# Performance work log

Measured on AMD Instinct MI355X. Metric: run time of the kernel, lower is better.

## Reference

```python
import jax, jax.numpy as jnp
import numpy as np

ENC_IN = 21
D_MODEL = 512
E_LAYERS = 2
PRED_LEN = 96
SEQ_LEN = 512
BATCH = 128


def _gru_layer(x, W_ih, W_hh, b_ih, b_hh):
    # x: [B, T, F]; W_ih: [3d, F]; W_hh: [3d, d]; gate order r, z, n (PyTorch)
    B = x.shape[0]
    d = W_hh.shape[1]
    gates_x = jnp.einsum('btf,gf->btg', x, W_ih) + b_ih  # [B, T, 3d], input GEMM hoisted out of scan

    def step(h, gx):
        gh = h @ W_hh.T + b_hh                       # [B, 3d]
        xr, xz, xn = jnp.split(gx, 3, axis=-1)
        hr, hz, hn = jnp.split(gh, 3, axis=-1)
        r = jax.nn.sigmoid(xr + hr)
        z = jax.nn.sigmoid(xz + hz)
        n = jnp.tanh(xn + r * hn)
        h_new = (1.0 - z) * n + z * h
        return h_new, h_new

    h0 = jnp.zeros((B, d), x.dtype)
    _, hs = jax.lax.scan(step, h0, jnp.swapaxes(gates_x, 0, 1))  # [T, B, d]
    return jnp.swapaxes(hs, 0, 1)  # [B, T, d]


def setup_inputs() -> dict:
    key = jax.random.key(0)
    ks = jax.random.split(key, 16)
    s = 1.0 / np.sqrt(D_MODEL)
    inp = {
        'x_enc': jax.random.normal(ks[0], (BATCH, SEQ_LEN, ENC_IN), jnp.float32),
        'x_mark_enc': jax.random.normal(ks[1], (BATCH, SEQ_LEN, 4), jnp.float32),
        'x_dec': jax.random.normal(ks[2], (BATCH, 144, ENC_IN), jnp.float32),
        'x_mark_dec': jax.random.normal(ks[3], (BATCH, 144, 4), jnp.float32),
        # GRU layer 0 (input size ENC_IN)
        'W_ih0': jax.random.uniform(ks[4], (3 * D_MODEL, ENC_IN), jnp.float32, -s, s),
        'W_hh0': jax.random.uniform(ks[5], (3 * D_MODEL, D_MODEL), jnp.float32, -s, s),
        'b_ih0': jax.random.uniform(ks[6], (3 * D_MODEL,), jnp.float32, -s, s),
        'b_hh0': jax.random.uniform(ks[7], (3 * D_MODEL,), jnp.float32, -s, s),
        # GRU layer 1 (input size D_MODEL)
        'W_ih1': jax.random.uniform(ks[8], (3 * D_MODEL, D_MODEL), jnp.float32, -s, s),
        'W_hh1': jax.random.uniform(ks[9], (3 * D_MODEL, D_MODEL), jnp.float32, -s, s),
        'b_ih1': jax.random.uniform(ks[10], (3 * D_MODEL,), jnp.float32, -s, s),
        'b_hh1': jax.random.uniform(ks[11], (3 * D_MODEL,), jnp.float32, -s, s),
        # projection Linear(d_model -> enc_in)
        'W_proj': jax.random.uniform(ks[12], (ENC_IN, D_MODEL), jnp.float32, -s, s),
        'b_proj': jax.random.uniform(ks[13], (ENC_IN,), jnp.float32, -s, s),
    }
    return inp


def reference(x_enc, x_mark_enc, x_dec, x_mark_dec,
              W_ih0, W_hh0, b_ih0, b_hh0,
              W_ih1, W_hh1, b_ih1, b_hh1,
              W_proj, b_proj):
    h = _gru_layer(x_enc, W_ih0, W_hh0, b_ih0, b_hh0)
    h = _gru_layer(h, W_ih1, W_hh1, b_ih1, b_hh1)
    enc_out = jnp.einsum('btd,od->bto', h, W_proj) + b_proj  # [B, T, enc_in]
    return enc_out[:, -PRED_LEN:, :]
```

## Files before the change

### kernel.cpp

```cpp
#include <hip/hip_runtime.h>
#include <cmath>


#define TSEQ   512
#define NB     128
#define DM     512
#define ENCF   21
#define PREDL  96
#define TSTART 416
#define NTHR   256
#define NBLK   256

#define L_WHH0 0
#define L_WHH1 (24*DM)
#define L_HCH  (2*24*DM)
#define L_SC0  (L_HCH + 32*128)
#define L_SC1  (L_SC0 + 4*32*33)
#define L_BIA0 (L_SC1 + 4*32*33)
#define L_BIA1 (L_BIA0 + 48)
#define L_WIH0 (L_BIA1 + 48)
#define L_XCH  (L_WIH0 + 24*24)
#define L_WP   (L_XCH + 32*24)
#define L_HNT  (L_WP + 168)
#define LDS_FLOATS (L_HNT + 256)
#define LDS_BYTES  (LDS_FLOATS * 4)

#define SWZB(x) (((((x) & 1) << 2)) | ((((x) & 2)) << 3))

__device__ float g_h0A[NB * DM];
__device__ float g_h0B[NB * DM];
__device__ float g_h1A[NB * DM];
__device__ float g_h1B[NB * DM];
__device__ unsigned g_bar[16];

extern "C" __global__ void zero_bar_kernel() {
  if (threadIdx.x < 16)
    __hip_atomic_store(&g_bar[threadIdx.x], 0u, __ATOMIC_RELAXED, __HIP_MEMORY_SCOPE_AGENT);
}

__device__ __forceinline__ float sigf(float x) { return 1.0f / (1.0f + expf(-x)); }

union DF2 { double d; float2 f; };
__device__ __forceinline__ float2 ld2_dc(const float* p) {
  DF2 u; u.d = *(const volatile double*)p; return u.f;
}
__device__ __forceinline__ float ld_dc(const float* p) { return *(const volatile float*)p; }
__device__ __forceinline__ void st_dc(float* p, float v) { *(volatile float*)p = v; }

extern "C" __global__ __launch_bounds__(NTHR, 1)
void gru2_fused(const float* __restrict__ x_enc,
                const float* __restrict__ Wih0, const float* __restrict__ Whh0,
                const float* __restrict__ bih0, const float* __restrict__ bhh0,
                const float* __restrict__ Wih1, const float* __restrict__ Whh1,
                const float* __restrict__ bih1, const float* __restrict__ bhh1,
                const float* __restrict__ Wproj, const float* __restrict__ bproj,
                float* __restrict__ outp)
{
  extern __shared__ float lds[];

  const int tid = threadIdx.x;
  const int bid = blockIdx.x;
  const int bt  = bid & 3;
  const int jt  = bid >> 2;
  const int b0  = bt << 5;
  const int j0  = jt << 3;
  const int l   = tid & 63;
  const int wv  = tid >> 6;
  const int pr  = l & 3;
  const int pb4 = (l >> 2) & 3;
  const int kg  = l >> 4;

  const float2 z2 = make_float2(0.f, 0.f);

  for (int f = tid; f < 24 * 128; f += NTHR) {
    int r = f >> 7, w4 = f & 127;
    int R = ((r >> 3) << 9) + j0 + (r & 7);
    int dst = r * DM + ((w4 << 2) ^ SWZB(r));
    *(float4*)(lds + L_WHH0 + dst) = *(const float4*)(Whh0 + (size_t)R * DM + (w4 << 2));
    *(float4*)(lds + L_WHH1 + dst) = *(const float4*)(Whh1 + (size_t)R * DM + (w4 << 2));
  }
  for (int idx = tid; idx < 24 * ENCF; idx += NTHR) {
    int r = idx / ENCF, kx = idx - r * ENCF;
    int R = ((r >> 3) << 9) + j0 + (r & 7);
    lds[L_WIH0 + r * 24 + kx] = Wih0[R * ENCF + kx];
  }
  if (tid < 24) {
    int R = ((tid >> 3) << 9) + j0 + (tid & 7);
    lds[L_BIA0 + tid]      = bhh0[R];
    lds[L_BIA0 + 24 + tid] = bih0[R];
    lds[L_BIA1 + tid]      = bhh1[R];
    lds[L_BIA1 + 24 + tid] = bih1[R];
  }
  for (int idx = tid; idx < 21 * 8; idx += NTHR) {
    int o = idx >> 3, j = idx & 7;
    lds[L_WP + idx] = Wproj[o * DM + j0 + j];
  }

#pragma unroll 1
  for (int g = 0; g <= TSEQ; ++g) {
    const float* h0r = (g & 1) ? g_h0A : g_h0B;
    float*       h0w = (g & 1) ? g_h0B : g_h0A;
    const float* h1r = (g & 1) ? g_h1B : g_h1A;
    float*       h1w = (g & 1) ? g_h1A : g_h1B;

    const int gx = (g < TSEQ) ? g : (TSEQ - 1);
    float rx[3];
#pragma unroll
    for (int q = 0; q < 3; ++q) {
      int idx = tid + (q << 8);
      float v = 0.0f;
      if (idx < 32 * ENCF) {
        int row = idx / ENCF, kx = idx - row * ENCF;
        v = x_enc[((size_t)(b0 + row) * TSEQ + gx) * ENCF + kx];
      }
      rx[q] = v;
    }

    float accA[8][6], accX[8][6];
#pragma unroll
    for (int i = 0; i < 8; ++i)
#pragma unroll
      for (int m = 0; m < 6; ++m) { accA[i][m] = 0.0f; accX[i][m] = 0.0f; }

    float2 ph[8];
#pragma unroll
    for (int q = 0; q < 8; ++q) {
      int idx = tid + (q << 8);
      int row = idx >> 6, c2 = idx & 63;
      ph[q] = (g == 0) ? z2
            : ld2_dc(h0r + (size_t)(b0 + row) * DM + (c2 << 1));
    }

#pragma unroll 1
    for (int c = 0; c < 4; ++c) {
      __syncthreads();
#pragma unroll
      for (int q = 0; q < 8; ++q) {
        int idx = tid + (q << 8);
        int row = idx >> 6, cf = (idx & 63) << 1;
        *(float2*)(lds + L_HCH + row * 128 + (cf ^ SWZB(row))) = ph[q];
      }
      __syncthreads();
      if (c < 3) {
#pragma unroll
        for (int q = 0; q < 8; ++q) {
          int idx = tid + (q << 8);
          int row = idx >> 6, c2 = idx & 63;
          ph[q] = (g == 0) ? z2
                : ld2_dc(h0r + (size_t)(b0 + row) * DM + ((c + 1) << 7) + (c2 << 1));
        }
      }
      float4 wx[6][2];
#pragma unroll
      for (int m = 0; m < 6; ++m) {
        int r = pr + (m << 2);
        int R = ((r >> 3) << 9) + j0 + (r & 7);
#pragma unroll
        for (int q = 0; q < 2; ++q) {
          int ww = (wv << 3) + (kg << 1) + q;
          wx[m][q] = *(const float4*)(Wih1 + (size_t)R * DM + (((c << 5) + ww) << 2));
        }
      }
#pragma unroll
      for (int q = 0; q < 2; ++q) {
        int ww = (wv << 3) + (kg << 1) + q;
        int colf = ((c << 5) + ww) << 2;
        float4 wh[6];
#pragma unroll
        for (int m = 0; m < 6; ++m) {
          int r = pr + (m << 2);
          wh[m] = *(const float4*)(lds + L_WHH0 + r * DM + (colf ^ SWZB(r)));
        }
#pragma unroll
        for (int i = 0; i < 8; ++i) {
          int b = pb4 + (i << 2);
          float4 hv = *(const float4*)(lds + L_HCH + b * 128 + ((ww << 2) ^ SWZB(b)));
#pragma unroll
          for (int m = 0; m < 6; ++m) {
            accA[i][m] += hv.x * wh[m].x + hv.y * wh[m].y + hv.z * wh[m].z + hv.w * wh[m].w;
            accX[i][m] += hv.x * wx[m][q].x + hv.y * wx[m][q].y + hv.z * wx[m][q].z + hv.w * wx[m][q].w;
          }
        }
      }
    }

#pragma unroll
    for (int i = 0; i < 8; ++i)
#pragma unroll
      for (int m = 0; m < 6; ++m) {
        float a = accA[i][m]; a += __shfl_xor(a, 16); a += __shfl_xor(a, 32); accA[i][m] = a;
        float x = accX[i][m]; x += __shfl_xor(x, 16); x += __shfl_xor(x, 32); accX[i][m] = x;
      }
    if (kg == 0) {
#pragma unroll
      for (int i = 0; i < 8; ++i) {
        int b = pb4 + (i << 2);
        float* s0 = lds + L_SC0 + (wv * 32 + b) * 33;
        float* s1 = lds + L_SC1 + (wv * 32 + b) * 33;
#pragma unroll
        for (int m = 0; m < 6; ++m) {
          int r = pr + (m << 2);
          s0[r] = accA[i][m];
          s1[(m < 4) ? r : (r + 8)] = accX[i][m];
        }
      }
    }

#pragma unroll
    for (int q = 0; q < 8; ++q) {
      int idx = tid + (q << 8);
      int row = idx >> 6, c2 = idx & 63;
      ph[q] = (g <= 1) ? z2
            : ld2_dc(h1r + (size_t)(b0 + row) * DM + (c2 << 1));
    }
#pragma unroll
    for (int i = 0; i < 8; ++i)
#pragma unroll
      for (int m = 0; m < 6; ++m) accA[i][m] = 0.0f;

#pragma unroll 1
    for (int c = 0; c < 4; ++c) {
      __syncthreads();
#pragma unroll
      for (int q = 0; q < 8; ++q) {
        int idx = tid + (q << 8);
        int row = idx >> 6, cf = (idx & 63) << 1;
        *(float2*)(lds + L_HCH + row * 128 + (cf ^ SWZB(row))) = ph[q];
      }
      __syncthreads();
      if (c < 3) {
#pragma unroll
        for (int q = 0; q < 8; ++q) {
          int idx = tid + (q << 8);
          int row = idx >> 6, c2 = idx & 63;
          ph[q] = (g <= 1) ? z2
                : ld2_dc(h1r + (size_t)(b0 + row) * DM + ((c + 1) << 7) + (c2 << 1));
        }
      }
#pragma unroll
      for (int q = 0; q < 2; ++q) {
        int ww = (wv << 3) + (kg << 1) + q;
        int colf = ((c << 5) + ww) << 2;
        float4 wh[6];
#pragma unroll
        for (int m = 0; m < 6; ++m) {
          int r = pr + (m << 2);
          wh[m] = *(const float4*)(lds + L_WHH1 + r * DM + (colf ^ SWZB(r)));
        }
#pragma unroll
        for (int i = 0; i < 8; ++i) {
          int b = pb4 + (i << 2);
          float4 hv = *(const float4*)(lds + L_HCH + b * 128 + ((ww << 2) ^ SWZB(b)));
#pragma unroll
          for (int m = 0; m < 6; ++m)
            accA[i][m] += hv.x * wh[m].x + hv.y * wh[m].y + hv.z * wh[m].z + hv.w * wh[m].w;
        }
      }
    }

#pragma unroll
    for (int i = 0; i < 8; ++i)
#pragma unroll
      for (int m = 0; m < 6; ++m) {
        float a = accA[i][m]; a += __shfl_xor(a, 16); a += __shfl_xor(a, 32); accA[i][m] = a;
      }
    if (kg == 0) {
#pragma unroll
      for (int i = 0; i < 8; ++i) {
        int b = pb4 + (i << 2);
        float* s1 = lds + L_SC1 + (wv * 32 + b) * 33;
#pragma unroll
        for (int m = 0; m < 6; ++m) {
          int r = pr + (m << 2);
          if (m < 4) s1[r] += accA[i][m];
          else       s1[r]  = accA[i][m];
        }
      }
    }

#pragma unroll
    for (int q = 0; q < 3; ++q) {
      int idx = tid + (q << 8);
      if (idx < 32 * ENCF) {
        int row = idx / ENCF, kx = idx - row * ENCF;
        lds[L_XCH + row * 24 + kx] = rx[q];
      }
    }
    __syncthreads();

    {
      int b = tid >> 3, j = tid & 7;
      float sR0 = 0.f, sZ0 = 0.f, sN0 = 0.f;
      float sR1 = 0.f, sZ1 = 0.f, sN1h = 0.f, sN1x = 0.f;
#pragma unroll
      for (int w = 0; w < 4; ++w) {
        const float* s0 = lds + L_SC0 + (w * 32 + b) * 33;
        const float* s1 = lds + L_SC1 + (w * 32 + b) * 33;
        sR0 += s0[j]; sZ0 += s0[8 + j]; sN0 += s0[16 + j];
        sR1 += s1[j]; sZ1 += s1[8 + j]; sN1h += s1[16 + j]; sN1x += s1[24 + j];
      }
      size_t hix = (size_t)(b0 + b) * DM + j0 + j;
      if (g < TSEQ) {
        float xr = 0.f, xz = 0.f, xn = 0.f;
        const float* xrow = lds + L_XCH + b * 24;
#pragma unroll
        for (int k = 0; k < ENCF; ++k) {
          float xv = xrow[k];
          xr += xv * lds[L_WIH0 + j * 24 + k];
          xz += xv * lds[L_WIH0 + (8 + j) * 24 + k];
          xn += xv * lds[L_WIH0 + (16 + j) * 24 + k];
        }
        float h0prev = (g == 0) ? 0.f : ld_dc(h0r + hix);
        float r0 = sigf(xr + lds[L_BIA0 + 24 + j] + sR0 + lds[L_BIA0 + j]);
        float z0 = sigf(xz + lds[L_BIA0 + 32 + j] + sZ0 + lds[L_BIA0 + 8 + j]);
        float n0 = tanhf(xn + lds[L_BIA0 + 40 + j] + r0 * (sN0 + lds[L_BIA0 + 16 + j]));
        st_dc(h0w + hix, (1.0f - z0) * n0 + z0 * h0prev);
      }
      if (g >= 1) {
        float h1prev = (g == 1) ? 0.f : ld_dc(h1r + hix);
        float r1 = sigf(sR1 + lds[L_BIA1 + 24 + j] + lds[L_BIA1 + j]);
        float z1 = sigf(sZ1 + lds[L_BIA1 + 32 + j] + lds[L_BIA1 + 8 + j]);
        float n1 = tanhf(sN1x + lds[L_BIA1 + 40 + j] + r1 * (sN1h + lds[L_BIA1 + 16 + j]));
        float h1n = (1.0f - z1) * n1 + z1 * h1prev;
        st_dc(h1w + hix, h1n);
        lds[L_HNT + (b << 3) + j] = h1n;
      }
    }

    if (g >= TSTART + 1) {
      __syncthreads();
      int tp = g - 1 - TSTART;
#pragma unroll
      for (int q = 0; q < 3; ++q) {
        int idx = tid + (q << 8);
        if (idx < 32 * ENCF) {
          int b = idx / ENCF, o = idx - b * ENCF;
          const float* hb = lds + L_HNT + (b << 3);
          const float* wo = lds + L_WP + (o << 3);
          float v = hb[0] * wo[0] + hb[1] * wo[1] + hb[2] * wo[2] + hb[3] * wo[3]
                  + hb[4] * wo[4] + hb[5] * wo[5] + hb[6] * wo[6] + hb[7] * wo[7];
          if (jt == 0) v += bproj[o];
          atomicAdd(outp + ((size_t)(b0 + b) * PREDL + tp) * ENCF + o, v);
        }
      }
    }

    __syncthreads();
    if (tid == 0) {
      asm volatile("s_waitcnt vmcnt(0) lgkmcnt(0)" ::: "memory");
      __hip_atomic_fetch_add(&g_bar[bt], 1u, __ATOMIC_RELAXED, __HIP_MEMORY_SCOPE_AGENT);
      unsigned tgt = 64u * (unsigned)(g + 1);
      while (__hip_atomic_load(&g_bar[bt], __ATOMIC_RELAXED, __HIP_MEMORY_SCOPE_AGENT) < tgt)
        __builtin_amdgcn_s_sleep(2);
    }
    __syncthreads();
    asm volatile("" ::: "memory");
  }
}

extern "C" void kernel_launch(void* const* d_in, const int* in_sizes, int n_in,
                              void* d_out, int out_size, void* d_ws, size_t ws_size,
                              hipStream_t stream)
{
  (void)in_sizes; (void)n_in; (void)d_ws; (void)ws_size;
  const float* x_enc  = (const float*)d_in[0];
  const float* W_ih0  = (const float*)d_in[4];
  const float* W_hh0  = (const float*)d_in[5];
  const float* b_ih0  = (const float*)d_in[6];
  const float* b_hh0  = (const float*)d_in[7];
  const float* W_ih1  = (const float*)d_in[8];
  const float* W_hh1  = (const float*)d_in[9];
  const float* b_ih1  = (const float*)d_in[10];
  const float* b_hh1  = (const float*)d_in[11];
  const float* W_proj = (const float*)d_in[12];
  const float* b_proj = (const float*)d_in[13];
  float* outp = (float*)d_out;

  hipLaunchKernelGGL(zero_bar_kernel, dim3(1), dim3(64), 0, stream);
  hipMemsetAsync(d_out, 0, (size_t)out_size * sizeof(float), stream);

  hipFuncSetAttribute((const void*)gru2_fused,
                      hipFuncAttributeMaxDynamicSharedMemorySize, (int)LDS_BYTES);

  const float* a0 = x_enc;
  const float* a1 = W_ih0;  const float* a2 = W_hh0;
  const float* a3 = b_ih0;  const float* a4 = b_hh0;
  const float* a5 = W_ih1;  const float* a6 = W_hh1;
  const float* a7 = b_ih1;  const float* a8 = b_hh1;
  const float* a9 = W_proj; const float* a10 = b_proj;
  float* a11 = outp;
  void* args[] = { &a0,&a1,&a2,&a3,&a4,&a5,&a6,&a7,&a8,&a9,&a10,&a11 };

  hipError_t e = hipLaunchCooperativeKernel((const void*)gru2_fused,
                                            dim3(NBLK), dim3(NTHR), args,
                                            (unsigned)LDS_BYTES, stream);
  if (e != hipSuccess) {
    hipLaunchKernelGGL(gru2_fused, dim3(NBLK), dim3(NTHR), LDS_BYTES, stream,
                       x_enc, W_ih0, W_hh0, b_ih0, b_hh0,
                       W_ih1, W_hh1, b_ih1, b_hh1, W_proj, b_proj, outp);
  }
}
```

Before: 22.13 ms.

## Double threads per block, split batch rows across wave halves, prefetch both h states

Raises the block size from 256 to 512 threads. The extra waves split the 32 batch rows in half, so each thread keeps 4×6 accumulators instead of 8×6. The layer-0 and layer-1 hidden-state chunks and the previous-h values are now all loaded at the start of each step, overlapping their global latency with compute, and the volatile accesses become relaxed agent-scope atomics. The aim is more latency hiding per step of the persistent recurrent loop, at the cost of more register and sync pressure and idle threads in the elementwise phase.

```diff
diff --git a/kernel.cpp b/kernel.cpp
--- a/kernel.cpp
+++ b/kernel.cpp
@@ -8,7 +8,7 @@
 #define ENCF   21
 #define PREDL  96
 #define TSTART 416
-#define NTHR   256
+#define NTHR   512
 #define NBLK   256
 
 #define L_WHH0 0
@@ -40,14 +40,22 @@
 
 __device__ __forceinline__ float sigf(float x) { return 1.0f / (1.0f + expf(-x)); }
 
-union DF2 { double d; float2 f; };
 __device__ __forceinline__ float2 ld2_dc(const float* p) {
-  DF2 u; u.d = *(const volatile double*)p; return u.f;
-}
-__device__ __forceinline__ float ld_dc(const float* p) { return *(const volatile float*)p; }
-__device__ __forceinline__ void st_dc(float* p, float v) { *(volatile float*)p = v; }
-
-extern "C" __global__ __launch_bounds__(NTHR, 1)
+  unsigned long long v = __hip_atomic_load((unsigned long long*)p,
+                                           __ATOMIC_RELAXED, __HIP_MEMORY_SCOPE_AGENT);
+  union { unsigned long long u; float2 f; } cv; cv.u = v; return cv.f;
+}
+__device__ __forceinline__ float ld_dc(const float* p) {
+  unsigned v = __hip_atomic_load((unsigned*)p,
+                                 __ATOMIC_RELAXED, __HIP_MEMORY_SCOPE_AGENT);
+  union { unsigned u; float f; } cv; cv.u = v; return cv.f;
+}
+__device__ __forceinline__ void st_dc(float* p, float v) {
+  union { float f; unsigned u; } cv; cv.f = v;
+  __hip_atomic_store((unsigned*)p, cv.u, __ATOMIC_RELAXED, __HIP_MEMORY_SCOPE_AGENT);
+}
+
+extern "C" __global__ __launch_bounds__(NTHR)
 void gru2_fused(const float* __restrict__ x_enc,
                 const float* __restrict__ Wih0, const float* __restrict__ Whh0,
                 const float* __restrict__ bih0, const float* __restrict__ bhh0,
@@ -58,17 +66,19 @@
 {
   extern __shared__ float lds[];
 
-  const int tid = threadIdx.x;
-  const int bid = blockIdx.x;
-  const int bt  = bid & 3;
-  const int jt  = bid >> 2;
-  const int b0  = bt << 5;
-  const int j0  = jt << 3;
-  const int l   = tid & 63;
-  const int wv  = tid >> 6;
-  const int pr  = l & 3;
-  const int pb4 = (l >> 2) & 3;
-  const int kg  = l >> 4;
+  const int tid  = threadIdx.x;
+  const int bid  = blockIdx.x;
+  const int bt   = bid & 3;
+  const int jt   = bid >> 2;
+  const int b0   = bt << 5;
+  const int j0   = jt << 3;
+  const int l    = tid & 63;
+  const int wv   = tid >> 6;
+  const int wq   = wv & 3;
+  const int half = wv >> 2;
+  const int pr   = l & 3;
+  const int pb4  = (l >> 2) & 3;
+  const int kg   = l >> 4;
 
   const float2 z2 = make_float2(0.f, 0.f);
 
@@ -104,10 +114,10 @@
     float*       h1w = (g & 1) ? g_h1A : g_h1B;
 
     const int gx = (g < TSEQ) ? g : (TSEQ - 1);
-    float rx[3];
-#pragma unroll
-    for (int q = 0; q < 3; ++q) {
-      int idx = tid + (q << 8);
+    float rx[2];
+#pragma unroll
+    for (int q = 0; q < 2; ++q) {
+      int idx = tid + (q << 9);
       float v = 0.0f;
       if (idx < 32 * ENCF) {
         int row = idx / ENCF, kx = idx - row * ENCF;
@@ -115,39 +125,47 @@
       }
       rx[q] = v;
     }
-
-    float accA[8][6], accX[8][6];
-#pragma unroll
-    for (int i = 0; i < 8; ++i)
+    float h0prev = 0.f, h1prev = 0.f;
+    size_t hix = 0;
+    if (tid < 256) {
+      int b = tid >> 3, j = tid & 7;
+      hix = (size_t)(b0 + b) * DM + j0 + j;
+      if (g > 0) h0prev = ld_dc(h0r + hix);
+      if (g > 1) h1prev = ld_dc(h1r + hix);
+    }
+    float2 ph0[4], ph1[4];
+#pragma unroll
+    for (int q = 0; q < 4; ++q) {
+      int idx = tid + (q << 9);
+      int row = idx >> 6, c2 = idx & 63;
+      size_t off = (size_t)(b0 + row) * DM + (c2 << 1);
+      ph0[q] = (g == 0) ? z2 : ld2_dc(h0r + off);
+      ph1[q] = (g <= 1) ? z2 : ld2_dc(h1r + off);
+    }
+
+    float accA[4][6], accX[4][6];
+#pragma unroll
+    for (int i = 0; i < 4; ++i)
 #pragma unroll
       for (int m = 0; m < 6; ++m) { accA[i][m] = 0.0f; accX[i][m] = 0.0f; }
-
-    float2 ph[8];
-#pragma unroll
-    for (int q = 0; q < 8; ++q) {
-      int idx = tid + (q << 8);
-      int row = idx >> 6, c2 = idx & 63;
-      ph[q] = (g == 0) ? z2
-            : ld2_dc(h0r + (size_t)(b0 + row) * DM + (c2 << 1));
-    }
 
 #pragma unroll 1
     for (int c = 0; c < 4; ++c) {
       __syncthreads();
 #pragma unroll
-      for (int q = 0; q < 8; ++q) {
-        int idx = tid + (q << 8);
+      for (int q = 0; q < 4; ++q) {
+        int idx = tid + (q << 9);
         int row = idx >> 6, cf = (idx & 63) << 1;
-        *(float2*)(lds + L_HCH + row * 128 + (cf ^ SWZB(row))) = ph[q];
+        *(float2*)(lds + L_HCH + row * 128 + (cf ^ SWZB(row))) = ph0[q];
       }
       __syncthreads();
       if (c < 3) {
 #pragma unroll
-        for (int q = 0; q < 8; ++q) {
-          int idx = tid + (q << 8);
+        for (int q = 0; q < 4; ++q) {
+          int idx = tid + (q << 9);
           int row = idx >> 6, c2 = idx & 63;
-          ph[q] = (g == 0) ? z2
-                : ld2_dc(h0r + (size_t)(b0 + row) * DM + ((c + 1) << 7) + (c2 << 1));
+          ph0[q] = (g == 0) ? z2
+                 : ld2_dc(h0r + (size_t)(b0 + row) * DM + ((c + 1) << 7) + (c2 << 1));
         }
       }
       float4 wx[6][2];
@@ -157,13 +175,13 @@
         int R = ((r >> 3) << 9) + j0 + (r & 7);
 #pragma unroll
         for (int q = 0; q < 2; ++q) {
-          int ww = (wv << 3) + (kg << 1) + q;
+          int ww = (wq << 3) + (kg << 1) + q;
           wx[m][q] = *(const float4*)(Wih1 + (size_t)R * DM + (((c << 5) + ww) << 2));
         }
       }
 #pragma unroll
       for (int q = 0; q < 2; ++q) {
-        int ww = (wv << 3) + (kg << 1) + q;
+        int ww = (wq << 3) + (kg << 1) + q;
         int colf = ((c << 5) + ww) << 2;
         float4 wh[6];
 #pragma unroll
@@ -172,8 +190,8 @@
           wh[m] = *(const float4*)(lds + L_WHH0 + r * DM + (colf ^ SWZB(r)));
         }
 #pragma unroll
-        for (int i = 0; i < 8; ++i) {
-          int b = pb4 + (i << 2);
+        for (int i = 0; i < 4; ++i) {
+          int b = pb4 + (i << 2) + (half << 4);
           float4 hv = *(const float4*)(lds + L_HCH + b * 128 + ((ww << 2) ^ SWZB(b)));
 #pragma unroll
           for (int m = 0; m < 6; ++m) {
@@ -185,7 +203,7 @@
     }
 
 #pragma unroll
-    for (int i = 0; i < 8; ++i)
+    for (int i = 0; i < 4; ++i)
 #pragma unroll
       for (int m = 0; m < 6; ++m) {
         float a = accA[i][m]; a += __shfl_xor(a, 16); a += __shfl_xor(a, 32); accA[i][m] = a;
@@ -193,10 +211,10 @@
       }
     if (kg == 0) {
 #pragma unroll
-      for (int i = 0; i < 8; ++i) {
-        int b = pb4 + (i << 2);
-        float* s0 = lds + L_SC0 + (wv * 32 + b) * 33;
-        float* s1 = lds + L_SC1 + (wv * 32 + b) * 33;
+      for (int i = 0; i < 4; ++i) {
+        int b = pb4 + (i << 2) + (half << 4);
+        float* s0 = lds + L_SC0 + (wq * 32 + b) * 33;
+        float* s1 = lds + L_SC1 + (wq * 32 + b) * 33;
 #pragma unroll
         for (int m = 0; m < 6; ++m) {
           int r = pr + (m << 2);
@@ -207,14 +225,7 @@
     }
 
 #pragma unroll
-    for (int q = 0; q < 8; ++q) {
-      int idx = tid + (q << 8);
-      int row = idx >> 6, c2 = idx & 63;
-      ph[q] = (g <= 1) ? z2
-            : ld2_dc(h1r + (size_t)(b0 + row) * DM + (c2 << 1));
-    }
-#pragma unroll
-    for (int i = 0; i < 8; ++i)
+    for (int i = 0; i < 4; ++i)
 #pragma unroll
       for (int m = 0; m < 6; ++m) accA[i][m] = 0.0f;
 
@@ -222,24 +233,24 @@
     for (int c = 0; c < 4; ++c) {
       __syncthreads();
 #pragma unroll
-      for (int q = 0; q < 8; ++q) {
-        int idx = tid + (q << 8);
+      for (int q = 0; q < 4; ++q) {
+        int idx = tid + (q << 9);
         int row = idx >> 6, cf = (idx & 63) << 1;
-        *(float2*)(lds + L_HCH + row * 128 + (cf ^ SWZB(row))) = ph[q];
+        *(float2*)(lds + L_HCH + row * 128 + (cf ^ SWZB(row))) = ph1[q];
       }
       __syncthreads();
       if (c < 3) {
 #pragma unroll
-        for (int q = 0; q < 8; ++q) {
-          int idx = tid + (q << 8);
+        for (int q = 0; q < 4; ++q) {
+          int idx = tid + (q << 9);
           int row = idx >> 6, c2 = idx & 63;
-          ph[q] = (g <= 1) ? z2
-                : ld2_dc(h1r + (size_t)(b0 + row) * DM + ((c + 1) << 7) + (c2 << 1));
+          ph1[q] = (g <= 1) ? z2
+                 : ld2_dc(h1r + (size_t)(b0 + row) * DM + ((c + 1) << 7) + (c2 << 1));
         }
       }
 #pragma unroll
       for (int q = 0; q < 2; ++q) {
-        int ww = (wv << 3) + (kg << 1) + q;
+        int ww = (wq << 3) + (kg << 1) + q;
         int colf = ((c << 5) + ww) << 2;
         float4 wh[6];
 #pragma unroll
@@ -248,8 +259,8 @@
           wh[m] = *(const float4*)(lds + L_WHH1 + r * DM + (colf ^ SWZB(r)));
         }
 #pragma unroll
-        for (int i = 0; i < 8; ++i) {
-          int b = pb4 + (i << 2);
+        for (int i = 0; i < 4; ++i) {
+          int b = pb4 + (i << 2) + (half << 4);
           float4 hv = *(const float4*)(lds + L_HCH + b * 128 + ((ww << 2) ^ SWZB(b)));
 #pragma unroll
           for (int m = 0; m < 6; ++m)
@@ -259,16 +270,16 @@
     }
 
 #pragma unroll
-    for (int i = 0; i < 8; ++i)
+    for (int i = 0; i < 4; ++i)
 #pragma unroll
       for (int m = 0; m < 6; ++m) {
         float a = accA[i][m]; a += __shfl_xor(a, 16); a += __shfl_xor(a, 32); accA[i][m] = a;
       }
     if (kg == 0) {
 #pragma unroll
-      for (int i = 0; i < 8; ++i) {
-        int b = pb4 + (i << 2);
-        float* s1 = lds + L_SC1 + (wv * 32 + b) * 33;
+      for (int i = 0; i < 4; ++i) {
+        int b = pb4 + (i << 2) + (half << 4);
+        float* s1 = lds + L_SC1 + (wq * 32 + b) * 33;
 #pragma unroll
         for (int m = 0; m < 6; ++m) {
           int r = pr + (m << 2);
@@ -279,8 +290,8 @@
     }
 
 #pragma unroll
-    for (int q = 0; q < 3; ++q) {
-      int idx = tid + (q << 8);
+    for (int q = 0; q < 2; ++q) {
+      int idx = tid + (q << 9);
       if (idx < 32 * ENCF) {
         int row = idx / ENCF, kx = idx - row * ENCF;
         lds[L_XCH + row * 24 + kx] = rx[q];
@@ -288,7 +299,7 @@
     }
     __syncthreads();
 
-    {
+    if (tid < 256) {
       int b = tid >> 3, j = tid & 7;
       float sR0 = 0.f, sZ0 = 0.f, sN0 = 0.f;
       float sR1 = 0.f, sZ1 = 0.f, sN1h = 0.f, sN1x = 0.f;
@@ -299,7 +310,6 @@
         sR0 += s0[j]; sZ0 += s0[8 + j]; sN0 += s0[16 + j];
         sR1 += s1[j]; sZ1 += s1[8 + j]; sN1h += s1[16 + j]; sN1x += s1[24 + j];
       }
-      size_t hix = (size_t)(b0 + b) * DM + j0 + j;
       if (g < TSEQ) {
         float xr = 0.f, xz = 0.f, xn = 0.f;
         const float* xrow = lds + L_XCH + b * 24;
@@ -310,14 +320,12 @@
           xz += xv * lds[L_WIH0 + (8 + j) * 24 + k];
           xn += xv * lds[L_WIH0 + (16 + j) * 24 + k];
         }
-        float h0prev = (g == 0) ? 0.f : ld_dc(h0r + hix);
         float r0 = sigf(xr + lds[L_BIA0 + 24 + j] + sR0 + lds[L_BIA0 + j]);
         float z0 = sigf(xz + lds[L_BIA0 + 32 + j] + sZ0 + lds[L_BIA0 + 8 + j]);
         float n0 = tanhf(xn + lds[L_BIA0 + 40 + j] + r0 * (sN0 + lds[L_BIA0 + 16 + j]));
         st_dc(h0w + hix, (1.0f - z0) * n0 + z0 * h0prev);
       }
       if (g >= 1) {
-        float h1prev = (g == 1) ? 0.f : ld_dc(h1r + hix);
         float r1 = sigf(sR1 + lds[L_BIA1 + 24 + j] + lds[L_BIA1 + j]);
         float z1 = sigf(sZ1 + lds[L_BIA1 + 32 + j] + lds[L_BIA1 + 8 + j]);
         float n1 = tanhf(sN1x + lds[L_BIA1 + 40 + j] + r1 * (sN1h + lds[L_BIA1 + 16 + j]));
@@ -331,8 +339,8 @@
       __syncthreads();
       int tp = g - 1 - TSTART;
 #pragma unroll
-      for (int q = 0; q < 3; ++q) {
-        int idx = tid + (q << 8);
+      for (int q = 0; q < 2; ++q) {
+        int idx = tid + (q << 9);
         if (idx < 32 * ENCF) {
           int b = idx / ENCF, o = idx - b * ENCF;
           const float* hb = lds + L_HNT + (b << 3);
```

Result: no change. 22.39 ms (+1.2%).
